# Optimization experiments

Hardware: AMD Instinct MI355X
Metric: run time of the kernel (lower is better)

Reference implementation:

```python
import jax, jax.numpy as jnp
import numpy as np
from math import factorial as fac

LMAX = 3
NMAX = 3
RC = 6.0
UNIT = RC / 3.0  # atomic_unit = rc/3
NSPEC = 4
N_ATOMS = 1000000


def _nnl():
    # a_{n,l} = 1 / ((2l+1) * 2^(2n+l) * n! * (n+l)!); nnl = sqrt(a_n a_n')
    a = np.array([[1.0 / ((2 * l + 1) * 2 ** (2 * n + l) * fac(n) * fac(n + l))
                   for l in range(LMAX + 1)] for n in range(NMAX + 1)])
    return jnp.asarray(np.sqrt(a[None] * a[:, None]), jnp.float32)  # (n, n', L+1)


def _yr_yi():
    one = np.ones((LMAX + 1, LMAX + 1))
    Yr = 2 * np.tril(one) - np.eye(LMAX + 1)   # real parts: diag weight 1 (m=0), lower weight 2
    Yi = 2 * np.triu(one, 1)                   # imag parts: strict upper weight 2
    return jnp.asarray(Yr, jnp.float32), jnp.asarray(Yi, jnp.float32)


def _sh_single(v):
    # Solid harmonics r^l * Ylm for one atom, packed into a (L+1, L+1) matrix:
    # Re(Y_l^m) at [l, l-m] (m=0 on the diagonal), Im(Y_l^m) at [l-m, l].
    x, y, z = v[0], v[1], v[2]
    r2 = x * x + y * y + z * z
    re = {(0, 0): jnp.asarray(0.28209479177387814, v.dtype)}  # 1/sqrt(4*pi)
    im = {(0, 0): jnp.zeros((), v.dtype)}
    for l in range(1, LMAX + 1):
        cl = -float(np.sqrt((2 * l + 1) / (2.0 * l)))
        re[(l, l)] = cl * (x * re[(l - 1, l - 1)] - y * im[(l - 1, l - 1)])
        im[(l, l)] = cl * (x * im[(l - 1, l - 1)] + y * re[(l - 1, l - 1)])
        g = float(np.sqrt(2 * l + 1))
        re[(l, l - 1)] = g * z * re[(l - 1, l - 1)]
        im[(l, l - 1)] = g * z * im[(l - 1, l - 1)]
        for m in range(l - 1):
            a = float(np.sqrt((4 * l * l - 1) / (l * l - m * m)))
            b = float(np.sqrt(((l - 1) ** 2 - m * m) / (4.0 * (l - 1) ** 2 - 1)))
            re[(l, m)] = a * (z * re[(l - 1, m)] - b * r2 * re[(l - 2, m)])
            im[(l, m)] = a * (z * im[(l - 1, m)] - b * r2 * im[(l - 2, m)])
    Y = jnp.zeros((LMAX + 1, LMAX + 1), v.dtype)
    for l in range(LMAX + 1):
        for m in range(l + 1):
            Y = Y.at[l, l - m].set(re[(l, m)])
            if m > 0:
                Y = Y.at[l - m, l].set(im[(l, m)])
    return Y


def _radial(dist):
    # Exp(-0.5 d^2/unit^2) * PolyCut(rc): smooth radial with polynomial cutoff
    cut = jnp.where(dist < RC, (1.0 - dist / RC) ** 2, 0.0)
    return jnp.exp(-0.5 * dist * dist / (UNIT * UNIT)) * cut


def _forward(coo, numbers):
    xyz = coo / UNIT
    d = jnp.sqrt(jnp.sum(xyz * xyz, axis=-1))              # (N,)
    n = 2.0 * jnp.arange(NMAX + 1, dtype=coo.dtype)        # exponents 2n
    r = _radial(UNIT * d)                                   # (N,)
    f = r[None] * d[None] ** n[:, None]                     # (nmax+1, N)
    Y = jnp.moveaxis(jax.vmap(_sh_single)(xyz), 0, -1)      # (L+1, L+1, N)
    onehot = (numbers[None, :] == jnp.arange(NSPEC)[:, None]).astype(coo.dtype)  # (S, N)
    # species-grouped reduction of the radial x Ylm outer product (fused einsum)
    c = jnp.einsum('kn,abn,sn->skab', f, Y, onehot)         # (S, nmax+1, L+1, L+1)
    Yr, Yi = _yr_yi()
    # p[a,b,n,m,l] = sum_m' Re-part + Im-part of c_{b,m} c*_{a,n} power spectrum
    p1 = jnp.einsum('bmlj,anlj,lj->abnml', c, c, Yr)
    p2 = jnp.einsum('bmil,anil,il->abnml', c, c, Yi)
    p = (p1 + p2) * _nnl()[None, None]
    return p.reshape(-1)                                    # dim = S^2 (nmax+1)^2 (L+1) = 1024


def setup_inputs() -> dict:
    key = jax.random.key(0)
    k1, k2 = jax.random.split(key)
    coo = 3.0 * jax.random.normal(k1, (N_ATOMS, 3), dtype=jnp.float32)
    numbers = jax.random.randint(k2, (N_ATOMS,), 0, NSPEC)
    return {"coo": coo, "numbers": numbers}


def reference(coo, numbers):
    return _forward(coo, numbers)
```

## Files before the change

kernel.cpp:

```cpp
#include <hip/hip_runtime.h>
#include <hip/hip_bf16.h>


typedef short short8 __attribute__((ext_vector_type(8)));
typedef float f32x4 __attribute__((ext_vector_type(4)));

__device__ __forceinline__ short bfc(float x) {
    __hip_bfloat16 h = __float2bfloat16(x);
    short s; __builtin_memcpy(&s, &h, 2); return s;
}

#define SWZ(c, a) (((c) << 6) + ((a) ^ (((c) & 7) << 3)))

__global__ void __launch_bounds__(256) soap_accum(
    const float* __restrict__ coo, const int* __restrict__ numbers,
    int N, int nb, float* __restrict__ partials)
{
    __shared__ short lT[4][2][16][64];
    __shared__ float cred[4][256];

    const int lane = threadIdx.x & 63;
    const int w = threadIdx.x >> 6;
    const int g = lane >> 4;
    const int comp = lane & 15;

    short* lAw = &lT[w][0][0][0];
    short* lBw = &lT[w][1][0][0];

    const int sw = (comp & 7) << 3, cb = comp << 6;
    const short8* pA0 = (const short8*)&lAw[cb + (( 8 * g)      ^ sw)];
    const short8* pA1 = (const short8*)&lAw[cb + ((32 + 8 * g) ^ sw)];
    const short8* pB0 = (const short8*)&lBw[cb + (( 8 * g)      ^ sw)];
    const short8* pB1 = (const short8*)&lBw[cb + ((32 + 8 * g) ^ sw)];

    f32x4 acc = {0.f, 0.f, 0.f, 0.f};

    const int stride = nb * 256;
    for (int base = (blockIdx.x * 4 + w) * 64; base < N; base += stride) {
        int i = base + lane;
        int ic = i < N ? i : N - 1;
        float x = coo[3 * ic + 0] * 0.5f;
        float y = coo[3 * ic + 1] * 0.5f;
        float z = coo[3 * ic + 2] * 0.5f;
        int num = numbers[ic];

        float r2 = x * x + y * y + z * z;
        float ds = sqrtf(r2);
        float t = 1.f - ds * (1.f / 3.f);
        float cut = (ds < 3.f) ? t * t : 0.f;
        float r = __expf(-0.5f * r2) * cut;
        if (i >= N) r = 0.f;

        float f0 = r, f1 = r * r2, f2 = f1 * r2, f3 = f2 * r2;

        const float Y00 = 0.28209479177387814f;
        float re11 = -0.34549414947133550f * x;
        float im11 = -0.34549414947133550f * y;
        float re10 =  0.48860251190291992f * z;
        float re22 = -1.11803398874989490f * (x * re11 - y * im11);
        float im22 = -1.11803398874989490f * (x * im11 + y * re11);
        float re21 =  2.23606797749978970f * z * re11;
        float im21 =  2.23606797749978970f * z * im11;
        float re20 =  1.93649167310370850f * (z * re10 - 0.16286750396763996f * r2);
        float re33 = -1.08012344973464350f * (x * re22 - y * im22);
        float im33 = -1.08012344973464350f * (x * im22 + y * re22);
        float re32 =  2.64575131106459070f * z * re22;
        float im32 =  2.64575131106459070f * z * im22;
        float re31 =  2.09165006633518890f * (z * re21 - 0.44721359549995793f * r2 * re11);
        float im31 =  2.09165006633518890f * (z * im21 - 0.44721359549995793f * r2 * im11);
        float re30 =  1.97202659436653870f * (z * re20 - 0.51639777949432220f * r2 * re10);

        short yv[16];
        yv[0] = bfc(Y00);  yv[1] = bfc(im11); yv[2]  = bfc(im22); yv[3]  = bfc(im33);
        yv[4] = bfc(re11); yv[5] = bfc(re10); yv[6]  = bfc(im21); yv[7]  = bfc(im32);
        yv[8] = bfc(re22); yv[9] = bfc(re21); yv[10] = bfc(re20); yv[11] = bfc(im31);
        yv[12] = bfc(re33); yv[13] = bfc(re32); yv[14] = bfc(re31); yv[15] = bfc(re30);

        short h[4] = {bfc(f0), bfc(f1), bfc(f2), bfc(f3)};

#pragma unroll
        for (int c = 0; c < 16; ++c) {
            short fv = (num == (c >> 2)) ? h[c & 3] : (short)0;
            lAw[SWZ(c, lane)] = fv;
            lBw[SWZ(c, lane)] = yv[c];
        }

        short8 A0 = *pA0, A1 = *pA1, B0 = *pB0, B1 = *pB1;

        acc = __builtin_amdgcn_mfma_f32_16x16x32_bf16(A0, B0, acc, 0, 0, 0);
        acc = __builtin_amdgcn_mfma_f32_16x16x32_bf16(A1, B1, acc, 0, 0, 0);
    }

#pragma unroll
    for (int rr = 0; rr < 4; ++rr)
        cred[w][((lane >> 4) * 4 + rr) * 16 + (lane & 15)] = acc[rr];
    __syncthreads();

    int tt = threadIdx.x;
    partials[blockIdx.x * 256 + tt] =
        cred[0][tt] + cred[1][tt] + cred[2][tt] + cred[3][tt];
}

__global__ void __launch_bounds__(256) soap_reduce(
    const float* __restrict__ partials, int nb, float* __restrict__ p2)
{
    int t = threadIdx.x;
    float v = 0.f;
    for (int r = blockIdx.x; r < nb; r += 32)
        v += partials[r * 256 + t];
    p2[blockIdx.x * 256 + t] = v;
}

__global__ void __launch_bounds__(1024) soap_finalize(
    const float* __restrict__ p2, float* __restrict__ out)
{
    __shared__ float cs[256];
    int t = threadIdx.x;
    if (t < 256) {
        float v = 0.f;
#pragma unroll
        for (int b = 0; b < 32; ++b) v += p2[b * 256 + t];
        cs[t] = v;
    }
    __syncthreads();

    int l = t & 3, m = (t >> 2) & 3, n = (t >> 4) & 3, b = (t >> 6) & 3, a = (t >> 8) & 3;
    const float* cbm = &cs[(b * 4 + m) * 16];
    const float* can = &cs[(a * 4 + n) * 16];

    float v = 0.f;
    for (int j = 0; j <= l; ++j) {
        float wgt = (j == l) ? 1.f : 2.f;
        v += wgt * cbm[l * 4 + j] * can[l * 4 + j];
    }
    for (int i = 0; i < l; ++i)
        v += 2.f * cbm[i * 4 + l] * can[i * 4 + l];

    const float fact[7] = {1.f, 1.f, 2.f, 6.f, 24.f, 120.f, 720.f};
    float an = 1.0f / ((float)(2 * l + 1) * (float)(1 << (2 * n + l)) * fact[n] * fact[n + l]);
    float am = 1.0f / ((float)(2 * l + 1) * (float)(1 << (2 * m + l)) * fact[m] * fact[m + l]);
    out[t] = v * sqrtf(an * am);
}

extern "C" void kernel_launch(void* const* d_in, const int* in_sizes, int n_in,
                              void* d_out, int out_size, void* d_ws, size_t ws_size,
                              hipStream_t stream)
{
    const float* coo = (const float*)d_in[0];
    const int* numbers = (const int*)d_in[1];
    int N = in_sizes[1];

    float* p2 = (float*)d_ws;
    float* partials = p2 + 32 * 256;

    long cap = (long)(ws_size / 1024) - 33;
    int nb = (int)(cap < 32 ? 32 : (cap > 1024 ? 1024 : cap));

    hipLaunchKernelGGL(soap_accum, dim3(nb), dim3(256), 0, stream,
                       coo, numbers, N, nb, partials);
    hipLaunchKernelGGL(soap_reduce, dim3(32), dim3(256), 0, stream,
                       partials, nb, p2);
    hipLaunchKernelGGL(soap_finalize, dim3(1), dim3(1024), 0, stream,
                       p2, (float*)d_out);
}
```

Before: 19.11 us.

## Interleave A/B bf16 operands into packed 32-bit LDS words and raise grid cap

```diff
diff --git a/kernel.cpp b/kernel.cpp
--- a/kernel.cpp
+++ b/kernel.cpp
@@ -4,34 +4,32 @@
 
 typedef short short8 __attribute__((ext_vector_type(8)));
 typedef float f32x4 __attribute__((ext_vector_type(4)));
+typedef unsigned int uint4v __attribute__((ext_vector_type(4)));
 
-__device__ __forceinline__ short bfc(float x) {
+__device__ __forceinline__ unsigned short bfu(float x) {
     __hip_bfloat16 h = __float2bfloat16(x);
-    short s; __builtin_memcpy(&s, &h, 2); return s;
+    unsigned short s; __builtin_memcpy(&s, &h, 2); return s;
 }
-
-#define SWZ(c, a) (((c) << 6) + ((a) ^ (((c) & 7) << 3)))
 
 __global__ void __launch_bounds__(256) soap_accum(
     const float* __restrict__ coo, const int* __restrict__ numbers,
     int N, int nb, float* __restrict__ partials)
 {
-    __shared__ short lT[4][2][16][64];
-    __shared__ float cred[4][256];
+    __shared__ unsigned int lT[4][16][64];
 
     const int lane = threadIdx.x & 63;
     const int w = threadIdx.x >> 6;
     const int g = lane >> 4;
     const int comp = lane & 15;
 
-    short* lAw = &lT[w][0][0][0];
-    short* lBw = &lT[w][1][0][0];
+    unsigned int* lTw = &lT[w][0][0];
 
-    const int sw = (comp & 7) << 3, cb = comp << 6;
-    const short8* pA0 = (const short8*)&lAw[cb + (( 8 * g)      ^ sw)];
-    const short8* pA1 = (const short8*)&lAw[cb + ((32 + 8 * g) ^ sw)];
-    const short8* pB0 = (const short8*)&lBw[cb + (( 8 * g)      ^ sw)];
-    const short8* pB1 = (const short8*)&lBw[cb + ((32 + 8 * g) ^ sw)];
+    const unsigned t4 = (unsigned)((comp & 7) << 2);
+    const unsigned rb = (unsigned)(comp << 6);
+    const uint4v* q0p = (const uint4v*)&lTw[rb + (( 8u * g)      ^ t4)];
+    const uint4v* q1p = (const uint4v*)&lTw[rb + (( 8u * g + 4)  ^ t4)];
+    const uint4v* q2p = (const uint4v*)&lTw[rb + ((32u + 8u * g)     ^ t4)];
+    const uint4v* q3p = (const uint4v*)&lTw[rb + ((32u + 8u * g + 4) ^ t4)];
 
     f32x4 acc = {0.f, 0.f, 0.f, 0.f};
 
@@ -70,35 +68,50 @@
         float im31 =  2.09165006633518890f * (z * im21 - 0.44721359549995793f * r2 * im11);
         float re30 =  1.97202659436653870f * (z * re20 - 0.51639777949432220f * r2 * re10);
 
-        short yv[16];
-        yv[0] = bfc(Y00);  yv[1] = bfc(im11); yv[2]  = bfc(im22); yv[3]  = bfc(im33);
-        yv[4] = bfc(re11); yv[5] = bfc(re10); yv[6]  = bfc(im21); yv[7]  = bfc(im32);
-        yv[8] = bfc(re22); yv[9] = bfc(re21); yv[10] = bfc(re20); yv[11] = bfc(im31);
-        yv[12] = bfc(re33); yv[13] = bfc(re32); yv[14] = bfc(re31); yv[15] = bfc(re30);
+        unsigned short yb[16];
+        yb[0] = bfu(Y00);  yb[1] = bfu(im11); yb[2]  = bfu(im22); yb[3]  = bfu(im33);
+        yb[4] = bfu(re11); yb[5] = bfu(re10); yb[6]  = bfu(im21); yb[7]  = bfu(im32);
+        yb[8] = bfu(re22); yb[9] = bfu(re21); yb[10] = bfu(re20); yb[11] = bfu(im31);
+        yb[12] = bfu(re33); yb[13] = bfu(re32); yb[14] = bfu(re31); yb[15] = bfu(re30);
 
-        short h[4] = {bfc(f0), bfc(f1), bfc(f2), bfc(f3)};
+        unsigned short hb[4] = {bfu(f0), bfu(f1), bfu(f2), bfu(f3)};
 
 #pragma unroll
         for (int c = 0; c < 16; ++c) {
-            short fv = (num == (c >> 2)) ? h[c & 3] : (short)0;
-            lAw[SWZ(c, lane)] = fv;
-            lBw[SWZ(c, lane)] = yv[c];
+            unsigned v = ((unsigned)yb[c] << 16)
+                       | (unsigned)((num == (c >> 2)) ? hb[c & 3] : (unsigned short)0);
+            lTw[(c << 6) + (lane ^ ((c & 7) << 2))] = v;
         }
 
-        short8 A0 = *pA0, A1 = *pA1, B0 = *pB0, B1 = *pB1;
+        uint4v q0 = *q0p, q1 = *q1p, q2 = *q2p, q3 = *q3p;
+
+        short8 A0, B0, A1, B1;
+#pragma unroll
+        for (int e = 0; e < 4; ++e) {
+            A0[e]     = (short)(q0[e] & 0xffffu);
+            A0[4 + e] = (short)(q1[e] & 0xffffu);
+            B0[e]     = (short)(q0[e] >> 16);
+            B0[4 + e] = (short)(q1[e] >> 16);
+            A1[e]     = (short)(q2[e] & 0xffffu);
+            A1[4 + e] = (short)(q3[e] & 0xffffu);
+            B1[e]     = (short)(q2[e] >> 16);
+            B1[4 + e] = (short)(q3[e] >> 16);
+        }
 
         acc = __builtin_amdgcn_mfma_f32_16x16x32_bf16(A0, B0, acc, 0, 0, 0);
         acc = __builtin_amdgcn_mfma_f32_16x16x32_bf16(A1, B1, acc, 0, 0, 0);
     }
 
+    float* credw = (float*)&lT[w][0][0];
 #pragma unroll
     for (int rr = 0; rr < 4; ++rr)
-        cred[w][((lane >> 4) * 4 + rr) * 16 + (lane & 15)] = acc[rr];
+        credw[((lane >> 4) * 4 + rr) * 16 + (lane & 15)] = acc[rr];
     __syncthreads();
 
     int tt = threadIdx.x;
     partials[blockIdx.x * 256 + tt] =
-        cred[0][tt] + cred[1][tt] + cred[2][tt] + cred[3][tt];
+        ((float*)&lT[0][0][0])[tt] + ((float*)&lT[1][0][0])[tt] +
+        ((float*)&lT[2][0][0])[tt] + ((float*)&lT[3][0][0])[tt];
 }
 
 __global__ void __launch_bounds__(256) soap_reduce(
@@ -154,7 +167,7 @@
     float* partials = p2 + 32 * 256;
 
     long cap = (long)(ws_size / 1024) - 33;
-    int nb = (int)(cap < 32 ? 32 : (cap > 1024 ? 1024 : cap));
+    int nb = (int)(cap < 32 ? 32 : (cap > 2048 ? 2048 : cap));
 
     hipLaunchKernelGGL(soap_accum, dim3(nb), dim3(256), 0, stream,
                        coo, numbers, N, nb, partials);
```

Measured after the change: 21.89 us. 14.6% more time.
